# Performance work log

Measured on AMD Instinct MI355X. Metric: run time of the kernel, lower is better.

## Reference

```python
import jax, jax.numpy as jnp
import numpy as np

# Module hyperparameters (from init_kwargs)
WH, WW = 8, 8            # window_size
H_RES, W_RES = 64, 64    # input_resolution
DIM = 256
NH = 1                   # num_heads hardcoded to 1 in the module
N = WH * WW              # tokens per window = 64
SCALE = (DIM // NH) ** -0.5
B = 64                   # theta_max batch
NW = (H_RES // WH) * (W_RES // WW)   # 64 windows
B_TOT = B * NW           # 4096


def _rel_coords():
    ch = np.arange(WH)
    cw = np.arange(WW)
    yy, xx = np.meshgrid(ch, cw, indexing='ij')
    flat = np.stack([yy.ravel(), xx.ravel()])          # (2, N)
    rel = flat[:, :, None] - flat[:, None, :]          # (2, N, N), values in [-(W-1), W-1]
    return rel[0], rel[1]                               # radius (rows), azimuth (cols)

RADIUS, AZIMUTH = _rel_coords()
# torch negative indexing wraps: idx -k -> table_size - k
AZ_IDX = jnp.asarray(np.mod(AZIMUTH, 2 * WW - 1))      # (N, N) into a_p/b_p (size 2*Ww-1)
R_IDX = jnp.asarray(np.mod(RADIUS, 2 * WH - 1))        # (N, N) into a_r/b_r (size 2*Wh-1)
AZ_ANG = jnp.asarray(AZIMUTH, jnp.float32) * (2.0 * np.pi / W_RES)  # azimuth * 2pi / W
RAD_F = jnp.asarray(RADIUS, jnp.float32)


def setup_inputs() -> dict:
    key = jax.random.key(0)
    ks = jax.random.split(key, 9)
    return {
        'x': jax.random.normal(ks[0], (B_TOT, N, DIM), jnp.float32),
        'theta_max': jax.random.uniform(ks[1], (B,), jnp.float32) * np.float32(np.pi),
        'qkv_w': jax.random.normal(ks[2], (DIM, 3 * DIM), jnp.float32) * 0.02,
        'qkv_b': jnp.zeros((3 * DIM,), jnp.float32),
        'proj_w': jax.random.normal(ks[3], (DIM, DIM), jnp.float32) * 0.02,
        'proj_b': jnp.zeros((DIM,), jnp.float32),
        'a_p': jax.random.normal(ks[4], (2 * WW - 1, NH), jnp.float32) * 0.02,
        'b_p': jax.random.normal(ks[5], (2 * WW - 1, NH), jnp.float32) * 0.02,
        'a_r': jax.random.normal(ks[6], (2 * WH - 1, NH), jnp.float32) * 0.02,
        'b_r': jax.random.normal(ks[7], (2 * WH - 1, NH), jnp.float32) * 0.02,
    }


def reference(x, theta_max, qkv_w, qkv_b, proj_w, proj_b, a_p, b_p, a_r, b_r):
    B_, Nn, C = x.shape
    # qkv projection -> (3, B_, nh, N, hd)
    qkv = (x @ qkv_w + qkv_b).reshape(B_, Nn, 3, NH, C // NH).transpose(2, 0, 3, 1, 4)
    q, k, v = qkv[0] * SCALE, qkv[1], qkv[2]
    attn = jnp.einsum('bhid,bhjd->bhij', q, k)          # (B_, nh, N, N)

    # azimuth (phi) bias: small-table gather + trig, shared across batch
    A_phi = a_p[AZ_IDX] * jnp.cos(AZ_ANG)[..., None] + b_p[AZ_IDX] * jnp.sin(AZ_ANG)[..., None]  # (N, N, nh)
    A_phi = jnp.transpose(A_phi, (2, 0, 1))[None]       # (1, nh, N, N)

    # radius (theta) bias: per-batch theta_max scaling
    tm = jnp.repeat(theta_max, B_ // theta_max.shape[0])                # (B_,)
    rn = RAD_F[None, :, :, None] * (tm[:, None, None, None] / H_RES)    # (B_, N, N, 1)
    A_th = a_r[R_IDX][None] * jnp.cos(rn) + b_r[R_IDX][None] * jnp.sin(rn)  # (B_, N, N, nh)
    A_th = jnp.transpose(A_th, (0, 3, 1, 2))            # (B_, nh, N, N)

    attn = jax.nn.softmax(attn + A_phi + A_th, axis=-1)
    out = jnp.einsum('bhij,bhjd->bhid', attn, v)        # (B_, nh, N, hd)
    out = out.transpose(0, 2, 1, 3).reshape(B_, Nn, C)
    return out @ proj_w + proj_b
```

## Files before the change

kernel.cpp:

```cpp
#include <hip/hip_runtime.h>
#include <hip/hip_bf16.h>


typedef __attribute__((ext_vector_type(8))) short short8;
typedef __attribute__((ext_vector_type(4))) float f32x4;

__device__ __forceinline__ unsigned short f2bf(float f) {
    f = fmaxf(f, -3.0e38f);
    f = fminf(f, 3.0e38f);
    __hip_bfloat16 h = __float2bfloat16(f);
    return *reinterpret_cast<unsigned short*>(&h);
}
__device__ __forceinline__ float sane(float f) {
    f = fmaxf(f, -1.0e10f);
    return fminf(f, 1.0e10f);
}

__global__ void prep_all(const float* __restrict__ qkv_w,
                         const float* __restrict__ proj_w,
                         const float* __restrict__ theta_max,
                         const float* __restrict__ a_p,
                         const float* __restrict__ b_p,
                         const float* __restrict__ a_r,
                         const float* __restrict__ b_r,
                         unsigned short* __restrict__ wq_pack,
                         unsigned short* __restrict__ wp_pack,
                         float* __restrict__ btab) {
    int t = blockIdx.x * blockDim.x + threadIdx.x;
    if (t < 24576) {
        int lane = t & 63, kt = (t >> 6) & 7, nt = t >> 9;
        int k0 = kt * 32 + (lane >> 4) * 8;
        int n  = nt * 16 + (lane & 15);
        unsigned short* dst = wq_pack + t * 8;
        for (int j = 0; j < 8; ++j) dst[j] = f2bf(qkv_w[(k0 + j) * 768 + n]);
    } else if (t < 32768) {
        int t2 = t - 24576;
        int lane = t2 & 63, kt = (t2 >> 6) & 7, nt = t2 >> 9;
        int k0 = kt * 32 + (lane >> 4) * 8;
        int n  = nt * 16 + (lane & 15);
        unsigned short* dst = wp_pack + t2 * 8;
        for (int j = 0; j < 8; ++j) dst[j] = f2bf(proj_w[(k0 + j) * 256 + n]);
    } else {
        int idx = t - 32768;
        if (idx >= 64 * 4096) return;
        int tt = idx >> 12, ij = idx & 4095, i = ij >> 6, j = ij & 63;
        int ri = (i >> 3) - (j >> 3);
        int az = (i & 7) - (j & 7);
        int azi = az < 0 ? az + 15 : az;
        int rii = ri < 0 ? ri + 15 : ri;
        float ang = (float)az * (6.28318530717958647692f / 64.0f);
        float aphi = a_p[azi] * cosf(ang) + b_p[azi] * sinf(ang);
        float rn = (float)ri * theta_max[tt] * (1.0f / 64.0f);
        float ath = a_r[rii] * cosf(rn) + b_r[rii] * sinf(rn);
        btab[idx] = sane(aphi + ath);
    }
}

#define LDS_BYTES 106496

__global__ __launch_bounds__(1024, 1)
void wattn_main(const float* __restrict__ x,
                const float* __restrict__ qkv_b,
                const float* __restrict__ proj_b,
                const unsigned short* __restrict__ wq_pack,
                const unsigned short* __restrict__ wp_pack,
                const float* __restrict__ btab,
                float* __restrict__ out) {
    extern __shared__ char smem[];
    unsigned short* kbuf = (unsigned short*)smem;
    unsigned short* qbuf = kbuf + 16896;
    unsigned short* vt   = qbuf + 16896;
    unsigned short* xbuf = vt;
    float* pmaxs = (float*)(smem + 104448);
    float* psums = pmaxs + 256;
    float* rbuf  = (float*)smem;

    const int tid = threadIdx.x;
    const int w = tid >> 6, lane = tid & 63;
    const int g = lane >> 4, c = lane & 15;
    const int bid = blockIdx.x;
    const int b = (bid & 7) * 512 + (bid >> 3);
    const float* xb = x + (size_t)b * 16384;

    float4 xv[4];
#pragma unroll
    for (int i = 0; i < 4; ++i) {
        int ch = tid + i * 1024;
        xv[i] = *(const float4*)(xb + (ch >> 6) * 256 + (ch & 63) * 4);
    }
#pragma unroll
    for (int i = 0; i < 4; ++i) {
        int ch = tid + i * 1024;
        unsigned short* dst = xbuf + (ch >> 6) * 264 + (ch & 63) * 4;
        dst[0] = f2bf(xv[i].x); dst[1] = f2bf(xv[i].y);
        dst[2] = f2bf(xv[i].z); dst[3] = f2bf(xv[i].w);
    }
    __syncthreads();

    f32x4 acc[3][4];
#pragma unroll
    for (int nt = 0; nt < 3; ++nt)
#pragma unroll
        for (int mt = 0; mt < 4; ++mt)
            acc[nt][mt] = f32x4{0.f, 0.f, 0.f, 0.f};

#pragma unroll
    for (int q4 = 0; q4 < 4; ++q4) {
        short8 af[4][2];
#pragma unroll
        for (int mt = 0; mt < 4; ++mt)
#pragma unroll
            for (int k2 = 0; k2 < 2; ++k2)
                af[mt][k2] = *(const short8*)(xbuf + (mt * 16 + c) * 264 + (q4 * 2 + k2) * 32 + g * 8);
#pragma unroll
        for (int nt = 0; nt < 3; ++nt) {
            int ntg = w * 3 + nt;
            short8 bfr[2];
#pragma unroll
            for (int k2 = 0; k2 < 2; ++k2)
                bfr[k2] = *(const short8*)(wq_pack + ((size_t)(ntg * 8 + q4 * 2 + k2) * 64 + lane) * 8);
#pragma unroll
            for (int mt = 0; mt < 4; ++mt)
#pragma unroll
                for (int k2 = 0; k2 < 2; ++k2)
                    acc[nt][mt] = __builtin_amdgcn_mfma_f32_16x16x32_bf16(
                        af[mt][k2], bfr[k2], acc[nt][mt], 0, 0, 0);
        }
    }
    __syncthreads();

#pragma unroll
    for (int nt = 0; nt < 3; ++nt) {
        int ntg = w * 3 + nt;
        int col = ntg * 16 + c;
        float bias = sane(qkv_b[col]);
#pragma unroll
        for (int mt = 0; mt < 4; ++mt)
#pragma unroll
            for (int rr = 0; rr < 4; ++rr) {
                int row = mt * 16 + g * 4 + rr;
                float v = acc[nt][mt][rr] + bias;
                if (ntg < 16)       qbuf[row * 264 + col] = f2bf(v * 0.0625f);
                else if (ntg < 32)  kbuf[row * 264 + (col - 256)] = f2bf(v);
                else                vt[(col - 512) * 72 + row] = f2bf(v);
            }
    }
    __syncthreads();

    const int mtq = w >> 2, ntq = w & 3;
    const float* bt = btab + (size_t)(b >> 6) * 4096;
    float bias_r[4];
#pragma unroll
    for (int rr = 0; rr < 4; ++rr)
        bias_r[rr] = bt[(mtq * 16 + g * 4 + rr) * 64 + ntq * 16 + c];
    f32x4 sacc = f32x4{0.f, 0.f, 0.f, 0.f};
#pragma unroll
    for (int kt = 0; kt < 8; ++kt) {
        short8 aq = *(const short8*)(qbuf + (mtq * 16 + c) * 264 + kt * 32 + g * 8);
        short8 bk = *(const short8*)(kbuf + (ntq * 16 + c) * 264 + kt * 32 + g * 8);
        sacc = __builtin_amdgcn_mfma_f32_16x16x32_bf16(aq, bk, sacc, 0, 0, 0);
    }
    float mloc[4];
#pragma unroll
    for (int rr = 0; rr < 4; ++rr) {
        float s = sacc[rr] + bias_r[rr];
        sacc[rr] = s;
        float mx = s;
        mx = fmaxf(mx, __shfl_xor(mx, 1, 16));
        mx = fmaxf(mx, __shfl_xor(mx, 2, 16));
        mx = fmaxf(mx, __shfl_xor(mx, 4, 16));
        mx = fmaxf(mx, __shfl_xor(mx, 8, 16));
        mloc[rr] = mx;
    }
    if (c == 0)
#pragma unroll
        for (int rr = 0; rr < 4; ++rr)
            pmaxs[(mtq * 16 + g * 4 + rr) * 4 + ntq] = mloc[rr];
    __syncthreads();

    unsigned short* Pbuf = kbuf;
#pragma unroll
    for (int rr = 0; rr < 4; ++rr) {
        int row = mtq * 16 + g * 4 + rr;
        float m = fmaxf(fmaxf(pmaxs[row * 4 + 0], pmaxs[row * 4 + 1]),
                        fmaxf(pmaxs[row * 4 + 2], pmaxs[row * 4 + 3]));
        float p = __expf(sacc[rr] - m);
        float s = p;
        s += __shfl_xor(s, 1, 16);
        s += __shfl_xor(s, 2, 16);
        s += __shfl_xor(s, 4, 16);
        s += __shfl_xor(s, 8, 16);
        if (c == 0) psums[row * 4 + ntq] = s;
        Pbuf[row * 72 + ntq * 16 + c] = f2bf(p);
    }
    __syncthreads();

    f32x4 oacc[4];
#pragma unroll
    for (int mt = 0; mt < 4; ++mt) oacc[mt] = f32x4{0.f, 0.f, 0.f, 0.f};
#pragma unroll
    for (int kt = 0; kt < 2; ++kt) {
        short8 bv = *(const short8*)(vt + (w * 16 + c) * 72 + kt * 32 + g * 8);
#pragma unroll
        for (int mt = 0; mt < 4; ++mt) {
            short8 ap = *(const short8*)(Pbuf + (mt * 16 + c) * 72 + kt * 32 + g * 8);
            oacc[mt] = __builtin_amdgcn_mfma_f32_16x16x32_bf16(ap, bv, oacc[mt], 0, 0, 0);
        }
    }
    unsigned short* aobuf = qbuf;
#pragma unroll
    for (int mt = 0; mt < 4; ++mt)
#pragma unroll
        for (int rr = 0; rr < 4; ++rr) {
            int lr = g * 4 + rr, row = mt * 16 + lr;
            float l = psums[row * 4 + 0] + psums[row * 4 + 1]
                    + psums[row * 4 + 2] + psums[row * 4 + 3];
            float inv = 1.0f / l;
            aobuf[row * 264 + w * 16 + c] = f2bf(oacc[mt][rr] * inv);
        }
    __syncthreads();

    f32x4 pacc[4];
#pragma unroll
    for (int mt = 0; mt < 4; ++mt) pacc[mt] = f32x4{0.f, 0.f, 0.f, 0.f};
#pragma unroll
    for (int kt = 0; kt < 8; ++kt) {
        short8 bp = *(const short8*)(wp_pack + ((size_t)(w * 8 + kt) * 64 + lane) * 8);
#pragma unroll
        for (int mt = 0; mt < 4; ++mt) {
            short8 aa = *(const short8*)(aobuf + (mt * 16 + c) * 264 + kt * 32 + g * 8);
            pacc[mt] = __builtin_amdgcn_mfma_f32_16x16x32_bf16(aa, bp, pacc[mt], 0, 0, 0);
        }
    }
    __syncthreads();

    float pb = sane(proj_b[w * 16 + c]);
#pragma unroll
    for (int mt = 0; mt < 4; ++mt)
#pragma unroll
        for (int rr = 0; rr < 4; ++rr)
            rbuf[(mt * 16 + g * 4 + rr) * 260 + w * 16 + c] = pacc[mt][rr] + pb;
    __syncthreads();

    float* ob = out + (size_t)b * 16384;
#pragma unroll
    for (int i = 0; i < 4; ++i) {
        int ch = tid + i * 1024;
        float4 vv = *(const float4*)(rbuf + (ch >> 6) * 260 + (ch & 63) * 4);
        *(float4*)(ob + (ch >> 6) * 256 + (ch & 63) * 4) = vv;
    }
}

extern "C" void kernel_launch(void* const* d_in, const int* in_sizes, int n_in,
                              void* d_out, int out_size, void* d_ws, size_t ws_size,
                              hipStream_t stream) {
    const float* x      = (const float*)d_in[0];
    const float* theta  = (const float*)d_in[1];
    const float* qkv_w  = (const float*)d_in[2];
    const float* qkv_b  = (const float*)d_in[3];
    const float* proj_w = (const float*)d_in[4];
    const float* proj_b = (const float*)d_in[5];
    const float* a_p    = (const float*)d_in[6];
    const float* b_p    = (const float*)d_in[7];
    const float* a_r    = (const float*)d_in[8];
    const float* b_r    = (const float*)d_in[9];
    float* out = (float*)d_out;

    unsigned short* wq_pack = (unsigned short*)d_ws;
    unsigned short* wp_pack = wq_pack + 196608;
    float* btab = (float*)((char*)d_ws + 524288);

    prep_all<<<1152, 256, 0, stream>>>(qkv_w, proj_w, theta, a_p, b_p, a_r, b_r,
                                       wq_pack, wp_pack, btab);

    hipFuncSetAttribute(reinterpret_cast<const void*>(wattn_main),
                        hipFuncAttributeMaxDynamicSharedMemorySize, LDS_BYTES);
    wattn_main<<<4096, 1024, LDS_BYTES, stream>>>(x, qkv_b, proj_b, wq_pack, wp_pack, btab, out);
}
```

Before: 733.6 us.

## Fold Wq·Wkᵀ into one matrix so scores come from x directly, shrink blocks

Precomputes M = Wq·Wkᵀ·scale in the prep kernel, plus the bias cross terms, so each window computes T = x·M and then scores = T·xᵀ. This removes the separate Q and K projections, and the attention-score GEMM now reads x instead of K. Blocks go from 1024 to 512 threads with smaller LDS to allow several blocks per CU, and LDS layouts switch from padding to XOR swizzles. The bf16 rounding of the folded matrix and of T changes numerical error, and the bias terms for u and w add small per-token reductions.

Result: no change. 723.0 us (-1.4%).

```diff
diff --git a/kernel.cpp b/kernel.cpp
--- a/kernel.cpp
+++ b/kernel.cpp
@@ -3,7 +3,10 @@
 
 
 typedef __attribute__((ext_vector_type(8))) short short8;
+typedef __attribute__((ext_vector_type(4))) short short4v;
 typedef __attribute__((ext_vector_type(4))) float f32x4;
+
+#define SCALE_ATT 0.0625f
 
 __device__ __forceinline__ unsigned short f2bf(float f) {
     f = fmaxf(f, -3.0e38f);
@@ -11,38 +14,89 @@
     __hip_bfloat16 h = __float2bfloat16(f);
     return *reinterpret_cast<unsigned short*>(&h);
 }
+__device__ __forceinline__ float bf2f(unsigned short u) {
+    unsigned int b = ((unsigned int)u) << 16;
+    float f;
+    __builtin_memcpy(&f, &b, 4);
+    return f;
+}
 __device__ __forceinline__ float sane(float f) {
     f = fmaxf(f, -1.0e10f);
     return fminf(f, 1.0e10f);
 }
 
+#define SWX(r, c) ((r) * 256 + ((c) ^ (((r) & 7) << 3)))
+#define SWV(d, t) ((d) * 64 + ((t) ^ (((d) & 7) << 3)))
+#define SWR(r, c) ((r) * 256 + ((c) ^ (((r) & 7) << 2)))
+
 __global__ void prep_all(const float* __restrict__ qkv_w,
                          const float* __restrict__ proj_w,
+                         const float* __restrict__ qkv_b,
                          const float* __restrict__ theta_max,
                          const float* __restrict__ a_p,
                          const float* __restrict__ b_p,
                          const float* __restrict__ a_r,
                          const float* __restrict__ b_r,
-                         unsigned short* __restrict__ wq_pack,
+                         unsigned short* __restrict__ m_pack,
+                         unsigned short* __restrict__ wv_pack,
                          unsigned short* __restrict__ wp_pack,
+                         float* __restrict__ qb2,
+                         float* __restrict__ kb2,
                          float* __restrict__ btab) {
-    int t = blockIdx.x * blockDim.x + threadIdx.x;
-    if (t < 24576) {
-        int lane = t & 63, kt = (t >> 6) & 7, nt = t >> 9;
-        int k0 = kt * 32 + (lane >> 4) * 8;
-        int n  = nt * 16 + (lane & 15);
-        unsigned short* dst = wq_pack + t * 8;
-        for (int j = 0; j < 8; ++j) dst[j] = f2bf(qkv_w[(k0 + j) * 768 + n]);
-    } else if (t < 32768) {
-        int t2 = t - 24576;
+    __shared__ float sA[16][257];
+    __shared__ float sB[16][257];
+    const int blk = blockIdx.x, tid = threadIdx.x;
+    if (blk < 256) {
+        int bi = blk >> 4, bj = blk & 15;
+        int row = tid >> 4, seg = tid & 15;
+        const float* pa = qkv_w + (size_t)(bi * 16 + row) * 768 + seg * 16;
+        const float* pb = qkv_w + (size_t)(bj * 16 + row) * 768 + 256 + seg * 16;
+        for (int q = 0; q < 4; ++q) {
+            float4 va = *(const float4*)(pa + q * 4);
+            float4 vb = *(const float4*)(pb + q * 4);
+            int cc = seg * 16 + q * 4;
+            sA[row][cc + 0] = va.x; sA[row][cc + 1] = va.y;
+            sA[row][cc + 2] = va.z; sA[row][cc + 3] = va.w;
+            sB[row][cc + 0] = vb.x; sB[row][cc + 1] = vb.y;
+            sB[row][cc + 2] = vb.z; sB[row][cc + 3] = vb.w;
+        }
+        __syncthreads();
+        int i = tid >> 4, n = tid & 15;
+        float d = 0.f;
+        for (int dq = 0; dq < 256; ++dq) d = fmaf(sA[i][dq], sB[n][dq], d);
+        int a = bi * 16 + i;
+        int nt = bj, kt = a >> 5, lane = ((a >> 3) & 3) * 16 + n, j = a & 7;
+        m_pack[(size_t)((nt * 8 + kt) * 64 + lane) * 8 + j] = f2bf(d * SCALE_ATT);
+    } else if (blk == 256) {
+        float s = 0.f;
+        for (int dq = 0; dq < 256; ++dq)
+            s = fmaf(qkv_w[(size_t)tid * 768 + dq], qkv_b[256 + dq], s);
+        qb2[tid] = s * SCALE_ATT;
+        if (tid == 0) {
+            float cc = 0.f;
+            for (int dq = 0; dq < 256; ++dq)
+                cc = fmaf(qkv_b[dq], qkv_b[256 + dq], cc);
+            qb2[256] = cc * SCALE_ATT;
+        }
+    } else if (blk == 257) {
+        float s = 0.f;
+        for (int dq = 0; dq < 256; ++dq)
+            s = fmaf(qkv_w[(size_t)tid * 768 + 256 + dq], qkv_b[dq], s);
+        kb2[tid] = s * SCALE_ATT;
+    } else if (blk < 290) {
+        int t2 = (blk - 258) * 256 + tid;
         int lane = t2 & 63, kt = (t2 >> 6) & 7, nt = t2 >> 9;
-        int k0 = kt * 32 + (lane >> 4) * 8;
-        int n  = nt * 16 + (lane & 15);
-        unsigned short* dst = wp_pack + t2 * 8;
-        for (int j = 0; j < 8; ++j) dst[j] = f2bf(proj_w[(k0 + j) * 256 + n]);
+        int k0 = kt * 32 + (lane >> 4) * 8, n = nt * 16 + (lane & 15);
+        unsigned short* dst = wv_pack + (size_t)t2 * 8;
+        for (int j = 0; j < 8; ++j) dst[j] = f2bf(qkv_w[(size_t)(k0 + j) * 768 + 512 + n]);
+    } else if (blk < 322) {
+        int t2 = (blk - 290) * 256 + tid;
+        int lane = t2 & 63, kt = (t2 >> 6) & 7, nt = t2 >> 9;
+        int k0 = kt * 32 + (lane >> 4) * 8, n = nt * 16 + (lane & 15);
+        unsigned short* dst = wp_pack + (size_t)t2 * 8;
+        for (int j = 0; j < 8; ++j) dst[j] = f2bf(proj_w[(size_t)(k0 + j) * 256 + n]);
     } else {
-        int idx = t - 32768;
-        if (idx >= 64 * 4096) return;
+        int idx = (blk - 322) * 256 + tid;
         int tt = idx >> 12, ij = idx & 4095, i = ij >> 6, j = ij & 63;
         int ri = (i >> 3) - (j >> 3);
         int az = (i & 7) - (j & 7);
@@ -56,23 +110,27 @@
     }
 }
 
-#define LDS_BYTES 106496
-
-__global__ __launch_bounds__(1024, 1)
+#define LDS_BYTES 76288
+
+__global__ __launch_bounds__(512, 4)
 void wattn_main(const float* __restrict__ x,
                 const float* __restrict__ qkv_b,
                 const float* __restrict__ proj_b,
-                const unsigned short* __restrict__ wq_pack,
+                const unsigned short* __restrict__ m_pack,
+                const unsigned short* __restrict__ wv_pack,
                 const unsigned short* __restrict__ wp_pack,
+                const float* __restrict__ qb2,
+                const float* __restrict__ kb2,
                 const float* __restrict__ btab,
                 float* __restrict__ out) {
     extern __shared__ char smem[];
-    unsigned short* kbuf = (unsigned short*)smem;
-    unsigned short* qbuf = kbuf + 16896;
-    unsigned short* vt   = qbuf + 16896;
-    unsigned short* xbuf = vt;
-    float* pmaxs = (float*)(smem + 104448);
-    float* psums = pmaxs + 256;
+    unsigned short* xb16 = (unsigned short*)smem;
+    unsigned short* tb16 = xb16 + 16384;
+    unsigned short* Pb   = xb16 + 32768;
+    float* uarr  = (float*)(smem + 74752);
+    float* warr  = uarr + 64;
+    float* pmaxs = uarr + 128;
+    float* psums = uarr + 256;
     float* rbuf  = (float*)smem;
 
     const int tid = threadIdx.x;
@@ -82,28 +140,103 @@
     const int b = (bid & 7) * 512 + (bid >> 3);
     const float* xb = x + (size_t)b * 16384;
 
-    float4 xv[4];
-#pragma unroll
-    for (int i = 0; i < 4; ++i) {
-        int ch = tid + i * 1024;
+    float4 xv[8];
+#pragma unroll
+    for (int i = 0; i < 8; ++i) {
+        int ch = tid + i * 512;
         xv[i] = *(const float4*)(xb + (ch >> 6) * 256 + (ch & 63) * 4);
     }
 #pragma unroll
-    for (int i = 0; i < 4; ++i) {
-        int ch = tid + i * 1024;
-        unsigned short* dst = xbuf + (ch >> 6) * 264 + (ch & 63) * 4;
-        dst[0] = f2bf(xv[i].x); dst[1] = f2bf(xv[i].y);
-        dst[2] = f2bf(xv[i].z); dst[3] = f2bf(xv[i].w);
-    }
-    __syncthreads();
-
-    f32x4 acc[3][4];
-#pragma unroll
-    for (int nt = 0; nt < 3; ++nt)
-#pragma unroll
-        for (int mt = 0; mt < 4; ++mt)
-            acc[nt][mt] = f32x4{0.f, 0.f, 0.f, 0.f};
-
+    for (int i = 0; i < 8; ++i) {
+        int ch = tid + i * 512;
+        short4v s4;
+        s4[0] = (short)f2bf(xv[i].x); s4[1] = (short)f2bf(xv[i].y);
+        s4[2] = (short)f2bf(xv[i].z); s4[3] = (short)f2bf(xv[i].w);
+        *(short4v*)(xb16 + SWX(ch >> 6, (ch & 63) * 4)) = s4;
+    }
+    __syncthreads();
+
+    {
+        int tok = tid >> 3, dc = tid & 7;
+        float su = 0.f, sw = 0.f;
+#pragma unroll
+        for (int j8 = 0; j8 < 4; ++j8) {
+            int d0 = dc * 32 + j8 * 8;
+            short8 xs = *(const short8*)(xb16 + SWX(tok, d0));
+#pragma unroll
+            for (int m = 0; m < 8; ++m) {
+                float xf = bf2f((unsigned short)xs[m]);
+                su = fmaf(xf, qb2[d0 + m], su);
+                sw = fmaf(xf, kb2[d0 + m], sw);
+            }
+        }
+        su += __shfl_xor(su, 1, 8); su += __shfl_xor(su, 2, 8); su += __shfl_xor(su, 4, 8);
+        sw += __shfl_xor(sw, 1, 8); sw += __shfl_xor(sw, 2, 8); sw += __shfl_xor(sw, 4, 8);
+        if (dc == 0) {
+            uarr[tok] = su + qb2[256];
+            warr[tok] = sw;
+        }
+    }
+
+    {
+        f32x4 tacc[2][4];
+#pragma unroll
+        for (int nt = 0; nt < 2; ++nt)
+#pragma unroll
+            for (int mt = 0; mt < 4; ++mt) tacc[nt][mt] = f32x4{0.f, 0.f, 0.f, 0.f};
+#pragma unroll
+        for (int q4 = 0; q4 < 4; ++q4) {
+            short8 af[4][2];
+#pragma unroll
+            for (int mt = 0; mt < 4; ++mt)
+#pragma unroll
+                for (int k2 = 0; k2 < 2; ++k2)
+                    af[mt][k2] = *(const short8*)(xb16 + SWX(mt * 16 + c, (q4 * 2 + k2) * 32 + g * 8));
+#pragma unroll
+            for (int nt = 0; nt < 2; ++nt) {
+                int ntg = w * 2 + nt;
+                short8 bfr[2];
+#pragma unroll
+                for (int k2 = 0; k2 < 2; ++k2)
+                    bfr[k2] = *(const short8*)(m_pack + ((size_t)(ntg * 8 + q4 * 2 + k2) * 64 + lane) * 8);
+#pragma unroll
+                for (int mt = 0; mt < 4; ++mt)
+#pragma unroll
+                    for (int k2 = 0; k2 < 2; ++k2)
+                        tacc[nt][mt] = __builtin_amdgcn_mfma_f32_16x16x32_bf16(
+                            af[mt][k2], bfr[k2], tacc[nt][mt], 0, 0, 0);
+            }
+        }
+#pragma unroll
+        for (int nt = 0; nt < 2; ++nt) {
+            int col = (w * 2 + nt) * 16 + c;
+#pragma unroll
+            for (int mt = 0; mt < 4; ++mt)
+#pragma unroll
+                for (int rr = 0; rr < 4; ++rr)
+                    tb16[SWX(mt * 16 + g * 4 + rr, col)] = f2bf(tacc[nt][mt][rr]);
+        }
+    }
+    __syncthreads();
+
+    const int mtq = w >> 1, nq = w & 1;
+    f32x4 sacc[2];
+    sacc[0] = f32x4{0.f, 0.f, 0.f, 0.f};
+    sacc[1] = f32x4{0.f, 0.f, 0.f, 0.f};
+#pragma unroll
+    for (int kt = 0; kt < 8; ++kt) {
+        short8 aq = *(const short8*)(tb16 + SWX(mtq * 16 + c, kt * 32 + g * 8));
+#pragma unroll
+        for (int n2 = 0; n2 < 2; ++n2) {
+            short8 bx = *(const short8*)(xb16 + SWX(nq * 32 + n2 * 16 + c, kt * 32 + g * 8));
+            sacc[n2] = __builtin_amdgcn_mfma_f32_16x16x32_bf16(aq, bx, sacc[n2], 0, 0, 0);
+        }
+    }
+    f32x4 vacc[2][4];
+#pragma unroll
+    for (int nt = 0; nt < 2; ++nt)
+#pragma unroll
+        for (int mt = 0; mt < 4; ++mt) vacc[nt][mt] = f32x4{0.f, 0.f, 0.f, 0.f};
 #pragma unroll
     for (int q4 = 0; q4 < 4; ++q4) {
         short8 af[4][2];
@@ -111,142 +244,146 @@
         for (int mt = 0; mt < 4; ++mt)
 #pragma unroll
             for (int k2 = 0; k2 < 2; ++k2)
-                af[mt][k2] = *(const short8*)(xbuf + (mt * 16 + c) * 264 + (q4 * 2 + k2) * 32 + g * 8);
-#pragma unroll
-        for (int nt = 0; nt < 3; ++nt) {
-            int ntg = w * 3 + nt;
+                af[mt][k2] = *(const short8*)(xb16 + SWX(mt * 16 + c, (q4 * 2 + k2) * 32 + g * 8));
+#pragma unroll
+        for (int nt = 0; nt < 2; ++nt) {
+            int ntg = w * 2 + nt;
             short8 bfr[2];
 #pragma unroll
             for (int k2 = 0; k2 < 2; ++k2)
-                bfr[k2] = *(const short8*)(wq_pack + ((size_t)(ntg * 8 + q4 * 2 + k2) * 64 + lane) * 8);
+                bfr[k2] = *(const short8*)(wv_pack + ((size_t)(ntg * 8 + q4 * 2 + k2) * 64 + lane) * 8);
 #pragma unroll
             for (int mt = 0; mt < 4; ++mt)
 #pragma unroll
                 for (int k2 = 0; k2 < 2; ++k2)
-                    acc[nt][mt] = __builtin_amdgcn_mfma_f32_16x16x32_bf16(
-                        af[mt][k2], bfr[k2], acc[nt][mt], 0, 0, 0);
-        }
-    }
-    __syncthreads();
-
-#pragma unroll
-    for (int nt = 0; nt < 3; ++nt) {
-        int ntg = w * 3 + nt;
-        int col = ntg * 16 + c;
-        float bias = sane(qkv_b[col]);
+                    vacc[nt][mt] = __builtin_amdgcn_mfma_f32_16x16x32_bf16(
+                        af[mt][k2], bfr[k2], vacc[nt][mt], 0, 0, 0);
+        }
+    }
+    const float* bt = btab + (size_t)(b >> 6) * 4096;
+    {
+        float mloc[4];
+#pragma unroll
+        for (int rr = 0; rr < 4; ++rr) {
+            int row = mtq * 16 + g * 4 + rr;
+            float uu = uarr[row];
+            float s0 = sacc[0][rr] + bt[row * 64 + nq * 32 + c] + uu + warr[nq * 32 + c];
+            float s1 = sacc[1][rr] + bt[row * 64 + nq * 32 + 16 + c] + uu + warr[nq * 32 + 16 + c];
+            sacc[0][rr] = s0; sacc[1][rr] = s1;
+            float mx = fmaxf(s0, s1);
+            mx = fmaxf(mx, __shfl_xor(mx, 1, 16));
+            mx = fmaxf(mx, __shfl_xor(mx, 2, 16));
+            mx = fmaxf(mx, __shfl_xor(mx, 4, 16));
+            mx = fmaxf(mx, __shfl_xor(mx, 8, 16));
+            mloc[rr] = mx;
+        }
+        if (c == 0)
+#pragma unroll
+            for (int rr = 0; rr < 4; ++rr)
+                pmaxs[(mtq * 16 + g * 4 + rr) * 2 + nq] = mloc[rr];
+    }
+    __syncthreads();
+
+    unsigned short* vt = tb16;
+#pragma unroll
+    for (int nt = 0; nt < 2; ++nt) {
+        int dim = (w * 2 + nt) * 16 + c;
+        float bias = sane(qkv_b[512 + dim]);
 #pragma unroll
         for (int mt = 0; mt < 4; ++mt)
 #pragma unroll
-            for (int rr = 0; rr < 4; ++rr) {
-                int row = mt * 16 + g * 4 + rr;
-                float v = acc[nt][mt][rr] + bias;
-                if (ntg < 16)       qbuf[row * 264 + col] = f2bf(v * 0.0625f);
-                else if (ntg < 32)  kbuf[row * 264 + (col - 256)] = f2bf(v);
-                else                vt[(col - 512) * 72 + row] = f2bf(v);
-            }
-    }
-    __syncthreads();
-
-    const int mtq = w >> 2, ntq = w & 3;
-    const float* bt = btab + (size_t)(b >> 6) * 4096;
-    float bias_r[4];
-#pragma unroll
-    for (int rr = 0; rr < 4; ++rr)
-        bias_r[rr] = bt[(mtq * 16 + g * 4 + rr) * 64 + ntq * 16 + c];
-    f32x4 sacc = f32x4{0.f, 0.f, 0.f, 0.f};
-#pragma unroll
-    for (int kt = 0; kt < 8; ++kt) {
-        short8 aq = *(const short8*)(qbuf + (mtq * 16 + c) * 264 + kt * 32 + g * 8);
-        short8 bk = *(const short8*)(kbuf + (ntq * 16 + c) * 264 + kt * 32 + g * 8);
-        sacc = __builtin_amdgcn_mfma_f32_16x16x32_bf16(aq, bk, sacc, 0, 0, 0);
-    }
-    float mloc[4];
-#pragma unroll
-    for (int rr = 0; rr < 4; ++rr) {
-        float s = sacc[rr] + bias_r[rr];
-        sacc[rr] = s;
-        float mx = s;
-        mx = fmaxf(mx, __shfl_xor(mx, 1, 16));
-        mx = fmaxf(mx, __shfl_xor(mx, 2, 16));
-        mx = fmaxf(mx, __shfl_xor(mx, 4, 16));
-        mx = fmaxf(mx, __shfl_xor(mx, 8, 16));
-        mloc[rr] = mx;
-    }
-    if (c == 0)
-#pragma unroll
-        for (int rr = 0; rr < 4; ++rr)
-            pmaxs[(mtq * 16 + g * 4 + rr) * 4 + ntq] = mloc[rr];
-    __syncthreads();
-
-    unsigned short* Pbuf = kbuf;
+            for (int rr = 0; rr < 4; ++rr)
+                vt[SWV(dim, mt * 16 + g * 4 + rr)] = f2bf(vacc[nt][mt][rr] + bias);
+    }
 #pragma unroll
     for (int rr = 0; rr < 4; ++rr) {
         int row = mtq * 16 + g * 4 + rr;
-        float m = fmaxf(fmaxf(pmaxs[row * 4 + 0], pmaxs[row * 4 + 1]),
-                        fmaxf(pmaxs[row * 4 + 2], pmaxs[row * 4 + 3]));
-        float p = __expf(sacc[rr] - m);
-        float s = p;
+        float m = fmaxf(pmaxs[row * 2], pmaxs[row * 2 + 1]);
+        float p0 = __expf(sacc[0][rr] - m);
+        float p1 = __expf(sacc[1][rr] - m);
+        float s = p0 + p1;
         s += __shfl_xor(s, 1, 16);
         s += __shfl_xor(s, 2, 16);
         s += __shfl_xor(s, 4, 16);
         s += __shfl_xor(s, 8, 16);
-        if (c == 0) psums[row * 4 + ntq] = s;
-        Pbuf[row * 72 + ntq * 16 + c] = f2bf(p);
-    }
-    __syncthreads();
-
-    f32x4 oacc[4];
-#pragma unroll
-    for (int mt = 0; mt < 4; ++mt) oacc[mt] = f32x4{0.f, 0.f, 0.f, 0.f};
+        if (c == 0) psums[row * 2 + nq] = s;
+        Pb[row * 72 + nq * 32 + c] = f2bf(p0);
+        Pb[row * 72 + nq * 32 + 16 + c] = f2bf(p1);
+    }
+    __syncthreads();
+
+    f32x4 oacc[4][2];
+#pragma unroll
+    for (int mt = 0; mt < 4; ++mt)
+#pragma unroll
+        for (int n2 = 0; n2 < 2; ++n2) oacc[mt][n2] = f32x4{0.f, 0.f, 0.f, 0.f};
 #pragma unroll
     for (int kt = 0; kt < 2; ++kt) {
-        short8 bv = *(const short8*)(vt + (w * 16 + c) * 72 + kt * 32 + g * 8);
+        short8 bv[2];
+#pragma unroll
+        for (int n2 = 0; n2 < 2; ++n2)
+            bv[n2] = *(const short8*)(vt + SWV(w * 32 + n2 * 16 + c, kt * 32 + g * 8));
 #pragma unroll
         for (int mt = 0; mt < 4; ++mt) {
-            short8 ap = *(const short8*)(Pbuf + (mt * 16 + c) * 72 + kt * 32 + g * 8);
-            oacc[mt] = __builtin_amdgcn_mfma_f32_16x16x32_bf16(ap, bv, oacc[mt], 0, 0, 0);
-        }
-    }
-    unsigned short* aobuf = qbuf;
+            short8 ap = *(const short8*)(Pb + (mt * 16 + c) * 72 + kt * 32 + g * 8);
+#pragma unroll
+            for (int n2 = 0; n2 < 2; ++n2)
+                oacc[mt][n2] = __builtin_amdgcn_mfma_f32_16x16x32_bf16(ap, bv[n2], oacc[mt][n2], 0, 0, 0);
+        }
+    }
+    unsigned short* ao = xb16;
 #pragma unroll
     for (int mt = 0; mt < 4; ++mt)
 #pragma unroll
         for (int rr = 0; rr < 4; ++rr) {
-            int lr = g * 4 + rr, row = mt * 16 + lr;
-            float l = psums[row * 4 + 0] + psums[row * 4 + 1]
-                    + psums[row * 4 + 2] + psums[row * 4 + 3];
-            float inv = 1.0f / l;
-            aobuf[row * 264 + w * 16 + c] = f2bf(oacc[mt][rr] * inv);
-        }
-    __syncthreads();
-
-    f32x4 pacc[4];
-#pragma unroll
-    for (int mt = 0; mt < 4; ++mt) pacc[mt] = f32x4{0.f, 0.f, 0.f, 0.f};
+            int row = mt * 16 + g * 4 + rr;
+            float inv = 1.0f / (psums[row * 2] + psums[row * 2 + 1]);
+#pragma unroll
+            for (int n2 = 0; n2 < 2; ++n2)
+                ao[SWX(row, w * 32 + n2 * 16 + c)] = f2bf(oacc[mt][n2][rr] * inv);
+        }
+    __syncthreads();
+
+    f32x4 pacc[2][4];
+#pragma unroll
+    for (int n2 = 0; n2 < 2; ++n2)
+#pragma unroll
+        for (int mt = 0; mt < 4; ++mt) pacc[n2][mt] = f32x4{0.f, 0.f, 0.f, 0.f};
 #pragma unroll
     for (int kt = 0; kt < 8; ++kt) {
-        short8 bp = *(const short8*)(wp_pack + ((size_t)(w * 8 + kt) * 64 + lane) * 8);
-#pragma unroll
-        for (int mt = 0; mt < 4; ++mt) {
-            short8 aa = *(const short8*)(aobuf + (mt * 16 + c) * 264 + kt * 32 + g * 8);
-            pacc[mt] = __builtin_amdgcn_mfma_f32_16x16x32_bf16(aa, bp, pacc[mt], 0, 0, 0);
-        }
-    }
-    __syncthreads();
-
-    float pb = sane(proj_b[w * 16 + c]);
-#pragma unroll
-    for (int mt = 0; mt < 4; ++mt)
-#pragma unroll
-        for (int rr = 0; rr < 4; ++rr)
-            rbuf[(mt * 16 + g * 4 + rr) * 260 + w * 16 + c] = pacc[mt][rr] + pb;
+        short8 aa[4];
+#pragma unroll
+        for (int mt = 0; mt < 4; ++mt)
+            aa[mt] = *(const short8*)(ao + SWX(mt * 16 + c, kt * 32 + g * 8));
+#pragma unroll
+        for (int n2 = 0; n2 < 2; ++n2) {
+            short8 bp = *(const short8*)(wp_pack + ((size_t)((w * 2 + n2) * 8 + kt) * 64 + lane) * 8);
+#pragma unroll
+            for (int mt = 0; mt < 4; ++mt)
+                pacc[n2][mt] = __builtin_amdgcn_mfma_f32_16x16x32_bf16(aa[mt], bp, pacc[n2][mt], 0, 0, 0);
+        }
+    }
+    __syncthreads();
+
+    {
+#pragma unroll
+        for (int n2 = 0; n2 < 2; ++n2) {
+            int col = (w * 2 + n2) * 16 + c;
+            float pb = sane(proj_b[col]);
+#pragma unroll
+            for (int mt = 0; mt < 4; ++mt)
+#pragma unroll
+                for (int rr = 0; rr < 4; ++rr)
+                    rbuf[SWR(mt * 16 + g * 4 + rr, col)] = pacc[n2][mt][rr] + pb;
+        }
+    }
     __syncthreads();
 
     float* ob = out + (size_t)b * 16384;
 #pragma unroll
-    for (int i = 0; i < 4; ++i) {
-        int ch = tid + i * 1024;
-        float4 vv = *(const float4*)(rbuf + (ch >> 6) * 260 + (ch & 63) * 4);
+    for (int i = 0; i < 8; ++i) {
+        int ch = tid + i * 512;
+        float4 vv = *(const float4*)(rbuf + SWR(ch >> 6, (ch & 63) * 4));
         *(float4*)(ob + (ch >> 6) * 256 + (ch & 63) * 4) = vv;
     }
 }
@@ -266,14 +403,20 @@
     const float* b_r    = (const float*)d_in[9];
     float* out = (float*)d_out;
 
-    unsigned short* wq_pack = (unsigned short*)d_ws;
-    unsigned short* wp_pack = wq_pack + 196608;
-    float* btab = (float*)((char*)d_ws + 524288);
-
-    prep_all<<<1152, 256, 0, stream>>>(qkv_w, proj_w, theta, a_p, b_p, a_r, b_r,
-                                       wq_pack, wp_pack, btab);
+    unsigned short* m_pack  = (unsigned short*)d_ws;
+    unsigned short* wv_pack = m_pack + 65536;
+    unsigned short* wp_pack = wv_pack + 65536;
+    float* qb2  = (float*)((char*)d_ws + 393216);
+    float* kb2  = (float*)((char*)d_ws + 395264);
+    float* btab = (float*)((char*)d_ws + 396288);
+
+    prep_all<<<1346, 256, 0, stream>>>(qkv_w, proj_w, qkv_b, theta,
+                                       a_p, b_p, a_r, b_r,
+                                       m_pack, wv_pack, wp_pack, qb2, kb2, btab);
 
     hipFuncSetAttribute(reinterpret_cast<const void*>(wattn_main),
                         hipFuncAttributeMaxDynamicSharedMemorySize, LDS_BYTES);
-    wattn_main<<<4096, 1024, LDS_BYTES, stream>>>(x, qkv_b, proj_b, wq_pack, wp_pack, btab, out);
-}
+    wattn_main<<<4096, 512, LDS_BYTES, stream>>>(x, qkv_b, proj_b,
+                                                 m_pack, wv_pack, wp_pack,
+                                                 qb2, kb2, btab, out);
+}
```
